# Kernel optimization log

Hardware: AMD Instinct MI355X
Metric: run time of the kernel (lower is better)

## Reference

```python
import jax, jax.numpy as jnp
import numpy as np

B, H, W, C = 2, 128, 128, 128
K = 3            # window_size
NB = K * K       # neighbor_count = 9
RP = 8           # relative_position_dim
HID = 128        # edge hidden = max(256//2, 128)
EIN = 3 * C + RP # edge_input_dim = 392
CLIP = 3.0
GEPS = 1e-06     # gate_eps
LNE = 1e-05      # LayerNorm eps


def _ln(x, g, b):
    m = x.mean(-1, keepdims=True)
    v = ((x - m) ** 2).mean(-1, keepdims=True)
    return (x - m) * jax.lax.rsqrt(v + LNE) * g + b


def setup_inputs() -> dict:
    key = jax.random.key(0)
    ks = jax.random.split(key, 12)
    f32 = jnp.float32
    inp = {
        'tokens': jax.random.normal(ks[0], (B, H, W, C), dtype=f32),
        'ln1_g': jnp.ones((C,), f32), 'ln1_b': jnp.zeros((C,), f32),
        'ln2_g': jnp.ones((C,), f32), 'ln2_b': jnp.zeros((C,), f32),
        'rel_pos': 0.02 * jax.random.normal(ks[1], (NB, RP), dtype=f32),
        'dW1': 0.01 * jax.random.normal(ks[2], (EIN, HID), dtype=f32),
        'db1': jnp.zeros((HID,), f32),
        'dW2': 0.01 * jax.random.normal(ks[3], (HID, 1), dtype=f32),
        'db2': jnp.zeros((1,), f32),
        'rW1': 0.01 * jax.random.normal(ks[4], (EIN, HID), dtype=f32),
        'rb1': jnp.zeros((HID,), f32),
        'rW2': 0.01 * jax.random.normal(ks[5], (HID, 1), dtype=f32),
        'rb2': jnp.zeros((1,), f32),
        'vW': 0.01 * jax.random.normal(ks[6], (C, C), dtype=f32),
        'vb': jnp.zeros((C,), f32),
        'oW': 0.01 * jax.random.normal(ks[7], (C, C), dtype=f32),
        'ob': jnp.zeros((C,), f32),
        'eml_gamma': jnp.asarray(0.1, f32),
        'eml_lam': jnp.asarray(1.0, f32),
        'eml_bias': jnp.asarray(-0.3, f32),
    }
    return inp


def _edge_mlp(x, W1, b1, W2, b2):
    h = jax.nn.gelu(jnp.einsum('blnd,dh->blnh', x, W1) + b1, approximate=False)
    return jnp.einsum('blnh,ho->blno', h, W2) + b2


def _forward(tokens, ln1_g, ln1_b, ln2_g, ln2_b, rel_pos, dW1, db1, dW2, db2,
             rW1, rb1, rW2, rb2, vW, vb, oW, ob, eml_gamma, eml_lam, eml_bias,
             warmup_eta=1.0):
    Bh, Hh, Wh, Ch = tokens.shape
    L = Hh * Wh
    normalized = _ln(tokens, ln1_g, ln1_b)
    flat = normalized.reshape(Bh, L, Ch)
    # Unfold(kernel=3, padding=1): gather 9 shifted views, then replicate torch's
    # reshape of the (C, 9)-ordered channel axis into (9, C).
    pad = jnp.pad(normalized, ((0, 0), (1, 1), (1, 1), (0, 0)))
    shifts = [pad[:, i:i + Hh, j:j + Wh, :] for i in range(K) for j in range(K)]
    nbhd = jnp.stack(shifts, axis=-1)                       # [B,H,W,C,9]
    nbhd = nbhd.reshape(Bh, L, Ch * NB).reshape(Bh, L, NB, Ch)  # torch reshape semantics
    center = jnp.broadcast_to(flat[:, :, None, :], nbhd.shape)
    rel = jnp.broadcast_to(rel_pos[None, None], (Bh, L, NB, rel_pos.shape[-1]))
    edge_features = jnp.concatenate([center, nbhd, center - nbhd, rel], axis=-1)
    drive = _edge_mlp(edge_features, dW1, db1, dW2, db2)[..., 0]        # [B,L,9]
    resistance = _edge_mlp(edge_features, rW1, rb1, rW2, rb2)[..., 0]   # [B,L,9]
    # EML unit (Ohm's-law style gate): clamp(eta*gamma*drive/(lambda*softplus(R)+eps)+bias)
    energy = jnp.clip(
        warmup_eta * (eml_gamma * drive) / (eml_lam * jax.nn.softplus(resistance) + GEPS)
        + eml_bias, -CLIP, CLIP)
    gate = jax.nn.sigmoid(energy)                                        # [B,L,9]
    values = jnp.einsum('blnc,cd->blnd', nbhd, vW) + vb                  # [B,L,9,C]
    gate_mass = jnp.maximum(gate.sum(axis=2), GEPS)                      # [B,L]
    message = jnp.einsum('bln,blnc->blc', gate, values) / gate_mass[..., None]
    update = (jnp.einsum('blc,cd->bld', message, oW) + ob).reshape(Bh, Hh, Wh, Ch)
    output = _ln(tokens + update, ln2_g, ln2_b)  # dropout is identity at eval
    return output


def reference(tokens, ln1_g, ln1_b, ln2_g, ln2_b, rel_pos, dW1, db1, dW2, db2,
              rW1, rb1, rW2, rb2, vW, vb, oW, ob, eml_gamma, eml_lam, eml_bias):
    return _forward(tokens, ln1_g, ln1_b, ln2_g, ln2_b, rel_pos, dW1, db1, dW2, db2,
                    rW1, rb1, rW2, rb2, vW, vb, oW, ob, eml_gamma, eml_lam, eml_bias)
```

## Files before the change

### kernel.cpp

```cpp
#include <hip/hip_runtime.h>


#define USHORT unsigned short
#define AW 152

typedef __attribute__((ext_vector_type(8)))  __bf16 v8bf;
typedef __attribute__((ext_vector_type(8)))  USHORT v8u;
typedef __attribute__((ext_vector_type(16))) float  v16f;

__device__ __forceinline__ USHORT f2bf(float f) {
    unsigned v; __builtin_memcpy(&v, &f, 4);
    v += 0x7FFFu + ((v >> 16) & 1u);
    return (USHORT)(v >> 16);
}

template <int C>
__device__ __forceinline__ float dpps(float x) {
    return __int_as_float(
        __builtin_amdgcn_update_dpp(0, __float_as_int(x), C, 0xf, 0xf, true));
}
__device__ __forceinline__ float red32half(float x) {
    x += dpps<0x111>(x);
    x += dpps<0x112>(x);
    x += dpps<0x114>(x);
    x += dpps<0x118>(x);
    x += dpps<0x142>(x);
    return x;
}
__device__ __forceinline__ float red64(float x) {
    x = red32half(x);
    x += dpps<0x143>(x);
    return x;
}
__device__ __forceinline__ float bcast63(float x) {
    return __int_as_float(__builtin_amdgcn_readlane(__float_as_int(x), 63));
}

__global__ __launch_bounds__(256) void k_setup(
    const float* __restrict__ tok, const float* __restrict__ ln1g,
    const float* __restrict__ ln1b,
    const float* __restrict__ dW1, const float* __restrict__ db1,
    const float* __restrict__ rW1, const float* __restrict__ rb1,
    const float* __restrict__ rel, const float* __restrict__ dW2,
    const float* __restrict__ rW2, const float* __restrict__ vW,
    const float* __restrict__ vb,  const float* __restrict__ oW,
    USHORT* __restrict__ norm,
    USHORT* __restrict__ WnTg, USHORT* __restrict__ WcTg, USHORT* __restrict__ VTg,
    float* __restrict__ preg, float* __restrict__ vboWg, float* __restrict__ w2g)
{
    const int blk = blockIdx.x, t = threadIdx.x;
    if (blk >= 354) {
        const int p = (blk - 354) * 4 + (t >> 6);
        const int lane = t & 63;
        const float2 x = ((const float2*)(tok + (size_t)p * 128))[lane];
        float s = x.x + x.y;
        for (int m = 1; m < 64; m <<= 1) s += __shfl_xor(s, m);
        const float mean = s * (1.f / 128.f);
        const float d0 = x.x - mean, d1 = x.y - mean;
        float q = d0 * d0 + d1 * d1;
        for (int m = 1; m < 64; m <<= 1) q += __shfl_xor(q, m);
        const float rstd = rsqrtf(q * (1.f / 128.f) + 1e-5f);
        const float2 gg = ((const float2*)ln1g)[lane], bb = ((const float2*)ln1b)[lane];
        ((unsigned*)norm)[(size_t)p * 64 + lane] =
            (unsigned)f2bf(d0 * rstd * gg.x + bb.x) |
            ((unsigned)f2bf(d1 * rstd * gg.y + bb.y) << 16);
        return;
    }
    if (blk < 72) {
        int idx = blk * 256 + t;
        int n = ((idx >> 4) * 7282) >> 16;
        int k = idx - n * 144;
        int r = k >> 4, tt = k & 15, c2 = r + 9 * tt;
        float acc = 0.f;
        if (c2 < 128)
            for (int j = 0; j < 128; ++j) acc += vW[c2 * 128 + j] * oW[j * 128 + n];
        VTg[idx] = f2bf(acc);
    } else if (blk < 216) {
        int idx = (blk - 72) * 256 + t;
        int n = ((idx >> 4) * 7282) >> 16;
        int k = idx - n * 144;
        int r = k >> 4, tt = k & 15, c2 = r + 9 * tt;
        int col = n & 127;
        const float* W = (n < 128) ? dW1 : rW1;
        float val = 0.f;
        if (c2 < 128) val = W[(128 + c2) * 128 + col] - W[(256 + c2) * 128 + col];
        WnTg[idx] = f2bf(val);
    } else if (blk < 344) {
        int idx = (blk - 216) * 256 + t;
        int n = idx >> 7, c = idx & 127, col = n & 127;
        const float* W = (n < 128) ? dW1 : rW1;
        WcTg[idx] = f2bf(W[c * 128 + col] + W[(256 + c) * 128 + col]);
    } else if (blk < 353) {
        int n2 = blk - 344; int h = t;
        float acc;
        if (h < 128) {
            acc = db1[h];
            for (int r = 0; r < 8; ++r) acc += rel[n2 * 8 + r] * dW1[(384 + r) * 128 + h];
        } else {
            int hh = h - 128;
            acc = rb1[hh];
            for (int r = 0; r < 8; ++r) acc += rel[n2 * 8 + r] * rW1[(384 + r) * 128 + hh];
        }
        preg[n2 * 256 + h] = acc;
    } else {
        if (t < 128) {
            float acc = 0.f;
            for (int j = 0; j < 128; ++j) acc += vb[j] * oW[j * 128 + t];
            vboWg[t] = acc;
            w2g[t] = dW2[t];
            w2g[128 + t] = rW2[t];
        }
    }
}

__device__ __forceinline__ void gather_load(
    uint2 (&pf)[9], const USHORT* __restrict__ nb,
    int n2, int y, int bI, int tid)
{
    const int x = tid >> 2, q = tid & 3;
    #pragma unroll
    for (int r = 0; r < 9; ++r) {
        int u = 2 * n2 + r;
        int n = (u >= 18) ? (u - 18) : ((u >= 9) ? (u - 9) : u);
        int v = n2 * 128 + r;
        int c0 = (v * 7282) >> 16;
        int dyq = (n * 22) >> 6;
        int dx = n - 3 * dyq - 1;
        int dy = dyq - 1;
        int sy = y + dy, sx = x + dx;
        bool ok = ((unsigned)sy < 128u) && ((unsigned)sx < 128u);
        int e0 = (c0 & ~1) + 4 * q;
        size_t gidx = ((size_t)((bI * 128 + (ok ? sy : 0)) * 128 + (ok ? sx : 0))) * 128 + e0;
        const unsigned* gp = (const unsigned*)nb + (gidx >> 1);
        unsigned dw0 = gp[0], dw1 = gp[1];
        pf[r].x = ok ? dw0 : 0u;
        pf[r].y = ok ? dw1 : 0u;
    }
}

__device__ __forceinline__ void gather_store(
    USHORT* __restrict__ Ash, const uint2 (&pf)[9], int n2, int tid)
{
    const int x = tid >> 2, q = tid & 3;
    #pragma unroll
    for (int r = 0; r < 9; ++r) {
        int v = n2 * 128 + r;
        int c0 = (v * 7282) >> 16;
        unsigned dw0 = pf[r].x, dw1 = pf[r].y;
        unsigned nxt = (unsigned)__shfl_down((int)dw0, 1);
        unsigned o0, o1;
        if (c0 & 1) { o0 = (dw0 >> 16) | (dw1 << 16); o1 = (dw1 >> 16) | (nxt << 16); }
        else        { o0 = dw0;                       o1 = dw1; }
        *(uint2*)(Ash + x * AW + 16 * r + 4 * q) = make_uint2(o0, o1);
    }
}

__global__ __launch_bounds__(512, 2) void k_edge(
    const float* __restrict__ tok, const float* __restrict__ ln2g,
    const float* __restrict__ ln2b, const USHORT* __restrict__ nb,
    const USHORT* __restrict__ WnTg, const USHORT* __restrict__ WcTg,
    const USHORT* __restrict__ VTg, const float* __restrict__ preg,
    const float* __restrict__ vboWg, const float* __restrict__ w2g,
    const float* __restrict__ db2p, const float* __restrict__ rb2p,
    const float* __restrict__ gmp, const float* __restrict__ lmp,
    const float* __restrict__ bip, const float* __restrict__ obp,
    float* __restrict__ out)
{
    extern __shared__ char smem[];
    USHORT* Wsh  = (USHORT*)smem;
    USHORT* Ash  = (USHORT*)(smem + 77824);
    USHORT* VTl  = (USHORT*)(smem + 116736);
    float*  w2L  = (float*)(smem + 155648);
    float*  dsum = (float*)(smem + 156672);
    float*  rsum = (float*)(smem + 157184);
    float*  gateL= (float*)(smem + 157696);
    float*  sgL  = (float*)(smem + 158208);
    float*  updF = (float*)smem;

    const int tid = threadIdx.x;
    const int lane = tid & 63, wave = tid >> 6, hi = lane >> 5, l31 = lane & 31;
    const int mw = wave & 1, nw = wave >> 1;
    const int blk = blockIdx.x;
    const int bI = blk >> 7;
    const int y = ((blk & 7) << 4) | ((blk >> 3) & 15);
    const int p0 = (bI * 128 + y) * 128;

    for (int i = tid; i < 4096; i += 512) {
        int n = i >> 4, kv = i & 15;
        *(v8u*)(Wsh + n * AW + kv * 8) = *(const v8u*)(WcTg + n * 128 + kv * 8);
    }
    for (int i = tid; i < 2048; i += 512) {
        int x = i >> 4, kv = i & 15;
        *(v8u*)(Ash + x * AW + kv * 8) = *(const v8u*)(nb + (size_t)(p0 + x) * 128 + kv * 8);
    }
    for (int i = tid; i < 2304; i += 512) {
        int n = (i * 3641) >> 16;
        int kv = i - n * 18;
        *(v8u*)(VTl + n * AW + kv * 8) = *(const v8u*)(VTg + n * 144 + kv * 8);
    }
    if (tid < 256) w2L[tid] = w2g[tid];
    if (tid < 128) { dsum[tid] = 0.f; rsum[tid] = 0.f; sgL[tid] = 0.f; }
    __syncthreads();

    v16f cp[2][2];
    #pragma unroll
    for (int a = 0; a < 2; ++a)
        for (int b = 0; b < 2; ++b)
            for (int e = 0; e < 16; ++e) cp[a][b][e] = 0.f;
    #pragma unroll
    for (int ks = 0; ks < 8; ++ks) {
        v8bf af0 = *(const v8bf*)(Ash + (mw * 64 + l31) * AW + ks * 16 + hi * 8);
        v8bf af1 = *(const v8bf*)(Ash + (mw * 64 + 32 + l31) * AW + ks * 16 + hi * 8);
        v8bf bf0 = *(const v8bf*)(Wsh + (nw * 64 + l31) * AW + ks * 16 + hi * 8);
        v8bf bf1 = *(const v8bf*)(Wsh + (nw * 64 + 32 + l31) * AW + ks * 16 + hi * 8);
        cp[0][0] = __builtin_amdgcn_mfma_f32_32x32x16_bf16(af0, bf0, cp[0][0], 0, 0, 0);
        cp[0][1] = __builtin_amdgcn_mfma_f32_32x32x16_bf16(af0, bf1, cp[0][1], 0, 0, 0);
        cp[1][0] = __builtin_amdgcn_mfma_f32_32x32x16_bf16(af1, bf0, cp[1][0], 0, 0, 0);
        cp[1][1] = __builtin_amdgcn_mfma_f32_32x32x16_bf16(af1, bf1, cp[1][1], 0, 0, 0);
    }
    __syncthreads();

    for (int i = tid; i < 4608; i += 512) {
        int n = (i * 3641) >> 16;
        int kv = i - n * 18;
        *(v8u*)(Wsh + n * AW + kv * 8) = *(const v8u*)(WnTg + n * 144 + kv * 8);
    }
    {
        uint2 pf0[9];
        gather_load(pf0, nb, 0, y, bI, tid);
        gather_store(Ash, pf0, 0, tid);
    }

    const float gmv = gmp[0], lmv = lmp[0], biv = bip[0];
    const float db2v = db2p[0], rb2v = rb2p[0];
    const float wv0 = w2L[nw * 64 + l31];
    const float wv1 = w2L[nw * 64 + 32 + l31];

    v16f acc3[2];
    #pragma unroll
    for (int a = 0; a < 2; ++a)
        for (int e = 0; e < 16; ++e) acc3[a][e] = 0.f;

    __syncthreads();

    for (int n2 = 0; n2 < 9; ++n2) {
        const float pv0 = preg[n2 * 256 + nw * 64 + l31];
        const float pv1 = preg[n2 * 256 + nw * 64 + 32 + l31];

        uint2 pf[9];
        if (n2 < 8) gather_load(pf, nb, n2 + 1, y, bI, tid);

        v16f acc[2][2];
        #pragma unroll
        for (int a = 0; a < 2; ++a)
            for (int b = 0; b < 2; ++b) acc[a][b] = cp[a][b];
        #pragma unroll
        for (int ks = 0; ks < 9; ++ks) {
            v8bf af0 = *(const v8bf*)(Ash + (mw * 64 + l31) * AW + ks * 16 + hi * 8);
            v8bf af1 = *(const v8bf*)(Ash + (mw * 64 + 32 + l31) * AW + ks * 16 + hi * 8);
            v8bf bf0 = *(const v8bf*)(Wsh + (nw * 64 + l31) * AW + ks * 16 + hi * 8);
            v8bf bf1 = *(const v8bf*)(Wsh + (nw * 64 + 32 + l31) * AW + ks * 16 + hi * 8);
            acc[0][0] = __builtin_amdgcn_mfma_f32_32x32x16_bf16(af0, bf0, acc[0][0], 0, 0, 0);
            acc[0][1] = __builtin_amdgcn_mfma_f32_32x32x16_bf16(af0, bf1, acc[0][1], 0, 0, 0);
            acc[1][0] = __builtin_amdgcn_mfma_f32_32x32x16_bf16(af1, bf0, acc[1][0], 0, 0, 0);
            acc[1][1] = __builtin_amdgcn_mfma_f32_32x32x16_bf16(af1, bf1, acc[1][1], 0, 0, 0);
        }
        #pragma unroll
        for (int mt = 0; mt < 2; ++mt) {
            float part[16];
            #pragma unroll
            for (int rr = 0; rr < 16; ++rr) {
                float h0 = acc[mt][0][rr] + pv0;
                float h1 = acc[mt][1][rr] + pv1;
                float s0 = __builtin_amdgcn_rcpf(1.f + __expf(-1.702f * h0));
                float s1 = __builtin_amdgcn_rcpf(1.f + __expf(-1.702f * h1));
                part[rr] = h0 * s0 * wv0 + h1 * s1 * wv1;
            }
            #pragma unroll
            for (int rr = 0; rr < 16; ++rr) part[rr] = red32half(part[rr]);
            if (l31 == 31) {
                float* tgt = (nw < 2) ? dsum : rsum;
                #pragma unroll
                for (int rr = 0; rr < 16; ++rr) {
                    int row = mw * 64 + mt * 32 + (rr & 3) + 8 * (rr >> 2) + 4 * hi;
                    atomicAdd(&tgt[row], part[rr]);
                }
            }
        }
        v16f P[2];
        #pragma unroll
        for (int a = 0; a < 2; ++a)
            for (int e = 0; e < 16; ++e) P[a][e] = 0.f;
        #pragma unroll
        for (int ks = 0; ks < 9; ++ks) {
            v8bf af0 = *(const v8bf*)(Ash + (mw * 64 + l31) * AW + ks * 16 + hi * 8);
            v8bf af1 = *(const v8bf*)(Ash + (mw * 64 + 32 + l31) * AW + ks * 16 + hi * 8);
            v8bf vf  = *(const v8bf*)(VTl + (nw * 32 + l31) * AW + ks * 16 + hi * 8);
            P[0] = __builtin_amdgcn_mfma_f32_32x32x16_bf16(af0, vf, P[0], 0, 0, 0);
            P[1] = __builtin_amdgcn_mfma_f32_32x32x16_bf16(af1, vf, P[1], 0, 0, 0);
        }
        __syncthreads();
        if (n2 < 8) gather_store(Ash, pf, n2 + 1, tid);
        if (tid < 128) {
            float d = dsum[tid] + db2v, rr = rsum[tid] + rb2v;
            float sp = fmaxf(rr, 0.f) + log1pf(__expf(-fabsf(rr)));
            float e = gmv * d / (lmv * sp + 1e-6f) + biv;
            e = fminf(fmaxf(e, -3.f), 3.f);
            float gt = 1.f / (1.f + __expf(-e));
            gateL[tid] = gt; sgL[tid] += gt;
            dsum[tid] = 0.f; rsum[tid] = 0.f;
        }
        __syncthreads();
        #pragma unroll
        for (int mt = 0; mt < 2; ++mt) {
            const float4* gq = (const float4*)&gateL[mw * 64 + mt * 32 + 4 * hi];
            float4 ga = gq[0], gb = gq[2], gc = gq[4], gd = gq[6];
            float gs[16] = {ga.x, ga.y, ga.z, ga.w, gb.x, gb.y, gb.z, gb.w,
                            gc.x, gc.y, gc.z, gc.w, gd.x, gd.y, gd.z, gd.w};
            #pragma unroll
            for (int rr = 0; rr < 16; ++rr) acc3[mt][rr] += gs[rr] * P[mt][rr];
        }
    }

    if (tid < 128) {
        float s = sgL[tid];
        float m = fmaxf(s, 1e-6f);
        dsum[tid] = 1.f / m;
        rsum[tid] = s / m;
    }
    __syncthreads();

    {
        const int colc = nw * 32 + l31;
        const float vbw = vboWg[colc], obv = obp[colc];
        #pragma unroll
        for (int mt = 0; mt < 2; ++mt) {
            const int base = mw * 64 + mt * 32 + 4 * hi;
            const float4* iq = (const float4*)&dsum[base];
            const float4* sq = (const float4*)&rsum[base];
            float4 ia = iq[0], ib = iq[2], ic = iq[4], id = iq[6];
            float4 sa = sq[0], sb = sq[2], sc = sq[4], sd = sq[6];
            float iv[16] = {ia.x, ia.y, ia.z, ia.w, ib.x, ib.y, ib.z, ib.w,
                            ic.x, ic.y, ic.z, ic.w, id.x, id.y, id.z, id.w};
            float sv[16] = {sa.x, sa.y, sa.z, sa.w, sb.x, sb.y, sb.z, sb.w,
                            sc.x, sc.y, sc.z, sc.w, sd.x, sd.y, sd.z, sd.w};
            #pragma unroll
            for (int rr = 0; rr < 16; ++rr) {
                int row = base + (rr & 3) + 8 * (rr >> 2);
                updF[row * 128 + colc] = acc3[mt][rr] * iv[rr] + vbw * sv[rr] + obv;
            }
        }
    }
    __syncthreads();

    const float g20 = ln2g[lane], g21 = ln2g[lane + 64];
    const float b20 = ln2b[lane], b21 = ln2b[lane + 64];
    for (int q2 = 0; q2 < 16; ++q2) {
        int p = wave * 16 + q2;
        size_t gp = (size_t)(p0 + p) * 128;
        float x0 = tok[gp + lane]      + updF[p * 128 + lane];
        float x1 = tok[gp + lane + 64] + updF[p * 128 + lane + 64];
        float mean = bcast63(red64(x0 + x1)) * (1.f / 128.f);
        float d0 = x0 - mean, d1 = x1 - mean;
        float rstd = rsqrtf(bcast63(red64(d0 * d0 + d1 * d1)) * (1.f / 128.f) + 1e-5f);
        out[gp + lane]      = d0 * rstd * g20 + b20;
        out[gp + lane + 64] = d1 * rstd * g21 + b21;
    }
}

extern "C" void kernel_launch(void* const* d_in, const int* in_sizes, int n_in,
                              void* d_out, int out_size, void* d_ws, size_t ws_size,
                              hipStream_t stream) {
    const float* tok  = (const float*)d_in[0];
    const float* ln1g = (const float*)d_in[1];
    const float* ln1b = (const float*)d_in[2];
    const float* ln2g = (const float*)d_in[3];
    const float* ln2b = (const float*)d_in[4];
    const float* rel  = (const float*)d_in[5];
    const float* dW1  = (const float*)d_in[6];
    const float* db1  = (const float*)d_in[7];
    const float* dW2  = (const float*)d_in[8];
    const float* db2  = (const float*)d_in[9];
    const float* rW1  = (const float*)d_in[10];
    const float* rb1  = (const float*)d_in[11];
    const float* rW2  = (const float*)d_in[12];
    const float* rb2  = (const float*)d_in[13];
    const float* vW   = (const float*)d_in[14];
    const float* vb   = (const float*)d_in[15];
    const float* oW   = (const float*)d_in[16];
    const float* ob   = (const float*)d_in[17];
    const float* gm   = (const float*)d_in[18];
    const float* lm   = (const float*)d_in[19];
    const float* bi   = (const float*)d_in[20];
    float* out = (float*)d_out;

    char* w = (char*)d_ws;
    USHORT* norm = (USHORT*)w; w += 8388608;
    USHORT* WnTg = (USHORT*)w; w += 73728;
    USHORT* WcTg = (USHORT*)w; w += 65536;
    USHORT* VTg  = (USHORT*)w; w += 36864;
    float*  preg = (float*)w;  w += 9216;
    float*  vboWg= (float*)w;  w += 512;
    float*  w2g  = (float*)w;  w += 1024;

    hipFuncSetAttribute((const void*)k_edge,
                        hipFuncAttributeMaxDynamicSharedMemorySize, 158720);

    hipLaunchKernelGGL(k_setup, dim3(8546), dim3(256), 0, stream,
                       tok, ln1g, ln1b, dW1, db1, rW1, rb1, rel, dW2, rW2,
                       vW, vb, oW, norm, WnTg, WcTg, VTg, preg, vboWg, w2g);
    hipLaunchKernelGGL(k_edge, dim3(256), dim3(512), 158720, stream,
                       tok, ln2g, ln2b, norm, WnTg, WcTg, VTg, preg, vboWg, w2g,
                       db2, rb2, gm, lm, bi, ob, out);
}
```

Baseline: 185.5 us.

## Replace LDS atomic row sums with partial slots and fuse value MFMA loop

Each wave now writes its per-row partial sums for the drive and resistance MLPs into its own LDS slot with float4 stores, and the gate step adds the two partials. This replaces 16 LDS atomicAdds per lane-31 thread and removes the per-iteration zeroing of the sums. The value projection MFMAs are interleaved into the same k-loop as the edge MLP MFMAs, so the A fragments are loaded once and the MFMA stream is denser. The cost is higher register pressure from the extra live accumulators, slightly more shared memory, and one extra barrier after the loop.

Result: slower. 189.2 us (+2.0%).

```diff
diff --git a/kernel.cpp b/kernel.cpp
--- a/kernel.cpp
+++ b/kernel.cpp
@@ -171,10 +171,10 @@
     USHORT* Ash  = (USHORT*)(smem + 77824);
     USHORT* VTl  = (USHORT*)(smem + 116736);
     float*  w2L  = (float*)(smem + 155648);
-    float*  dsum = (float*)(smem + 156672);
-    float*  rsum = (float*)(smem + 157184);
-    float*  gateL= (float*)(smem + 157696);
-    float*  sgL  = (float*)(smem + 158208);
+    float*  dP   = (float*)(smem + 156672);
+    float*  rP   = (float*)(smem + 157696);
+    float*  gateL= (float*)(smem + 158720);
+    float*  sgL  = (float*)(smem + 159232);
     float*  updF = (float*)smem;
 
     const int tid = threadIdx.x;
@@ -199,7 +199,7 @@
         *(v8u*)(VTl + n * AW + kv * 8) = *(const v8u*)(VTg + n * 144 + kv * 8);
     }
     if (tid < 256) w2L[tid] = w2g[tid];
-    if (tid < 128) { dsum[tid] = 0.f; rsum[tid] = 0.f; sgL[tid] = 0.f; }
+    if (tid < 128) sgL[tid] = 0.f;
     __syncthreads();
 
     v16f cp[2][2];
@@ -241,6 +241,8 @@
     for (int a = 0; a < 2; ++a)
         for (int e = 0; e < 16; ++e) acc3[a][e] = 0.f;
 
+    float* sumBase = ((nw < 2) ? dP : rP) + (nw & 1) * 128;
+
     __syncthreads();
 
     for (int n2 = 0; n2 < 9; ++n2) {
@@ -254,16 +256,23 @@
         #pragma unroll
         for (int a = 0; a < 2; ++a)
             for (int b = 0; b < 2; ++b) acc[a][b] = cp[a][b];
+        v16f P[2];
+        #pragma unroll
+        for (int a = 0; a < 2; ++a)
+            for (int e = 0; e < 16; ++e) P[a][e] = 0.f;
         #pragma unroll
         for (int ks = 0; ks < 9; ++ks) {
             v8bf af0 = *(const v8bf*)(Ash + (mw * 64 + l31) * AW + ks * 16 + hi * 8);
             v8bf af1 = *(const v8bf*)(Ash + (mw * 64 + 32 + l31) * AW + ks * 16 + hi * 8);
             v8bf bf0 = *(const v8bf*)(Wsh + (nw * 64 + l31) * AW + ks * 16 + hi * 8);
             v8bf bf1 = *(const v8bf*)(Wsh + (nw * 64 + 32 + l31) * AW + ks * 16 + hi * 8);
+            v8bf vf  = *(const v8bf*)(VTl + (nw * 32 + l31) * AW + ks * 16 + hi * 8);
             acc[0][0] = __builtin_amdgcn_mfma_f32_32x32x16_bf16(af0, bf0, acc[0][0], 0, 0, 0);
             acc[0][1] = __builtin_amdgcn_mfma_f32_32x32x16_bf16(af0, bf1, acc[0][1], 0, 0, 0);
             acc[1][0] = __builtin_amdgcn_mfma_f32_32x32x16_bf16(af1, bf0, acc[1][0], 0, 0, 0);
             acc[1][1] = __builtin_amdgcn_mfma_f32_32x32x16_bf16(af1, bf1, acc[1][1], 0, 0, 0);
+            P[0] = __builtin_amdgcn_mfma_f32_32x32x16_bf16(af0, vf, P[0], 0, 0, 0);
+            P[1] = __builtin_amdgcn_mfma_f32_32x32x16_bf16(af1, vf, P[1], 0, 0, 0);
         }
         #pragma unroll
         for (int mt = 0; mt < 2; ++mt) {
@@ -279,36 +288,26 @@
             #pragma unroll
             for (int rr = 0; rr < 16; ++rr) part[rr] = red32half(part[rr]);
             if (l31 == 31) {
-                float* tgt = (nw < 2) ? dsum : rsum;
-                #pragma unroll
-                for (int rr = 0; rr < 16; ++rr) {
-                    int row = mw * 64 + mt * 32 + (rr & 3) + 8 * (rr >> 2) + 4 * hi;
-                    atomicAdd(&tgt[row], part[rr]);
-                }
+                float* t0 = sumBase + ((mw * 2 + mt) * 2 + hi) * 16;
+                *(float4*)(t0 +  0) = make_float4(part[0],  part[1],  part[2],  part[3]);
+                *(float4*)(t0 +  4) = make_float4(part[4],  part[5],  part[6],  part[7]);
+                *(float4*)(t0 +  8) = make_float4(part[8],  part[9],  part[10], part[11]);
+                *(float4*)(t0 + 12) = make_float4(part[12], part[13], part[14], part[15]);
             }
-        }
-        v16f P[2];
-        #pragma unroll
-        for (int a = 0; a < 2; ++a)
-            for (int e = 0; e < 16; ++e) P[a][e] = 0.f;
-        #pragma unroll
-        for (int ks = 0; ks < 9; ++ks) {
-            v8bf af0 = *(const v8bf*)(Ash + (mw * 64 + l31) * AW + ks * 16 + hi * 8);
-            v8bf af1 = *(const v8bf*)(Ash + (mw * 64 + 32 + l31) * AW + ks * 16 + hi * 8);
-            v8bf vf  = *(const v8bf*)(VTl + (nw * 32 + l31) * AW + ks * 16 + hi * 8);
-            P[0] = __builtin_amdgcn_mfma_f32_32x32x16_bf16(af0, vf, P[0], 0, 0, 0);
-            P[1] = __builtin_amdgcn_mfma_f32_32x32x16_bf16(af1, vf, P[1], 0, 0, 0);
         }
         __syncthreads();
         if (n2 < 8) gather_store(Ash, pf, n2 + 1, tid);
         if (tid < 128) {
-            float d = dsum[tid] + db2v, rr = rsum[tid] + rb2v;
+            int w32 = tid & 31;
+            int slot = (((tid >> 6) * 2 + ((tid >> 5) & 1)) * 2 + ((w32 >> 2) & 1)) * 16
+                       + ((w32 & 3) | (((w32 >> 3) & 3) << 2));
+            float d = dP[slot] + dP[128 + slot] + db2v;
+            float rr = rP[slot] + rP[128 + slot] + rb2v;
             float sp = fmaxf(rr, 0.f) + log1pf(__expf(-fabsf(rr)));
             float e = gmv * d / (lmv * sp + 1e-6f) + biv;
             e = fminf(fmaxf(e, -3.f), 3.f);
             float gt = 1.f / (1.f + __expf(-e));
             gateL[tid] = gt; sgL[tid] += gt;
-            dsum[tid] = 0.f; rsum[tid] = 0.f;
         }
         __syncthreads();
         #pragma unroll
@@ -322,11 +321,12 @@
         }
     }
 
+    __syncthreads();
     if (tid < 128) {
         float s = sgL[tid];
         float m = fmaxf(s, 1e-6f);
-        dsum[tid] = 1.f / m;
-        rsum[tid] = s / m;
+        dP[tid] = 1.f / m;
+        rP[tid] = s / m;
     }
     __syncthreads();
 
@@ -336,8 +336,8 @@
         #pragma unroll
         for (int mt = 0; mt < 2; ++mt) {
             const int base = mw * 64 + mt * 32 + 4 * hi;
-            const float4* iq = (const float4*)&dsum[base];
-            const float4* sq = (const float4*)&rsum[base];
+            const float4* iq = (const float4*)&dP[base];
+            const float4* sq = (const float4*)&rP[base];
             float4 ia = iq[0], ib = iq[2], ic = iq[4], id = iq[6];
             float4 sa = sq[0], sb = sq[2], sc = sq[4], sd = sq[6];
             float iv[16] = {ia.x, ia.y, ia.z, ia.w, ib.x, ib.y, ib.z, ib.w,
@@ -404,12 +404,12 @@
     float*  w2g  = (float*)w;  w += 1024;
 
     hipFuncSetAttribute((const void*)k_edge,
-                        hipFuncAttributeMaxDynamicSharedMemorySize, 158720);
+                        hipFuncAttributeMaxDynamicSharedMemorySize, 159744);
 
     hipLaunchKernelGGL(k_setup, dim3(8546), dim3(256), 0, stream,
                        tok, ln1g, ln1b, dW1, db1, rW1, rb1, rel, dW2, rW2,
                        vW, vb, oW, norm, WnTg, WcTg, VTg, preg, vboWg, w2g);
-    hipLaunchKernelGGL(k_edge, dim3(256), dim3(512), 158720, stream,
+    hipLaunchKernelGGL(k_edge, dim3(256), dim3(512), 159744, stream,
                        tok, ln2g, ln2b, norm, WnTg, WcTg, VTg, preg, vboWg, w2g,
                        db2, rb2, gm, lm, bi, ob, out);
 }
```
